# Kernel optimization log

Measured on AMD Instinct MI355X. Metric: run time of the kernel, lower is better.

## Reference

```python
import jax, jax.numpy as jnp
import numpy as np
from jax import lax

H = 32  # input_size == hidden_size
NUM_CLASSES = 10


def setup_inputs() -> dict:
    key = jax.random.key(0)
    ks = jax.random.split(key, 12)
    s = 1.0 / np.sqrt(H)  # torch default uniform(-1/sqrt(H), 1/sqrt(H))
    u = lambda k, shape: jax.random.uniform(k, shape, jnp.float32, -s, s)
    return {
        "x": jax.random.normal(ks[0], (512, 2048, H), jnp.float32),
        "W_ih0": u(ks[1], (H, H)),
        "W_hh0": u(ks[2], (H, H)),
        "b_ih0": u(ks[3], (H,)),
        "b_hh0": u(ks[4], (H,)),
        "W_ih1": u(ks[5], (H, H)),
        "W_hh1": u(ks[6], (H, H)),
        "b_ih1": u(ks[7], (H,)),
        "b_hh1": u(ks[8], (H,)),
        "fc_w": u(ks[9], (NUM_CLASSES, H)),
        "fc_b": u(ks[10], (NUM_CLASSES,)),
    }


def reference(x, W_ih0, W_hh0, b_ih0, b_hh0, W_ih1, W_hh1, b_ih1, b_hh1, fc_w, fc_b):
    # x: [B, T, H]; 2-layer tanh RNN, return logits from final hidden of layer 2.
    B = x.shape[0]
    h0 = jnp.zeros((B, H), x.dtype)

    def step(carry, x_t):
        h1, h2 = carry
        h1 = jnp.tanh(x_t @ W_ih0.T + b_ih0 + h1 @ W_hh0.T + b_hh0)
        h2 = jnp.tanh(h1 @ W_ih1.T + b_ih1 + h2 @ W_hh1.T + b_hh1)
        return (h1, h2), None

    xT = jnp.swapaxes(x, 0, 1)  # [T, B, H] for scan over time
    (_, h2_final), _ = lax.scan(step, (h0, h0), xT)
    return h2_final @ fc_w.T + fc_b  # [B, NUM_CLASSES]
```

## Files before the change

kernel.cpp:

```cpp
#include <hip/hip_runtime.h>

#define RH 32
#define RT 2048
#define RB 512
#define RC 10

#define XRING 0
#define H1OFF 512
#define H2OFF 544
#define TRASH 576
#define LDSF  608

__device__ __forceinline__ float fast_tanh(float x) {
    float e = __builtin_amdgcn_exp2f(x * 2.88539008177792681472f);
    return fmaf(-2.0f, __builtin_amdgcn_rcpf(e + 1.0f), 1.0f);
}

__global__ __launch_bounds__(64) void rnn2_kernel(
    const float* __restrict__ x,
    const float* __restrict__ W_ih0, const float* __restrict__ W_hh0,
    const float* __restrict__ b_ih0, const float* __restrict__ b_hh0,
    const float* __restrict__ W_ih1, const float* __restrict__ W_hh1,
    const float* __restrict__ b_ih1, const float* __restrict__ b_hh1,
    const float* __restrict__ fc_w, const float* __restrict__ fc_b,
    float* __restrict__ out)
{
    __shared__ float lds[LDSF];
    const int b    = blockIdx.x;
    const int lane = threadIdx.x;
    const int j    = lane & 31;
    const int half = lane >> 5;

    const float* WA = half ? W_hh1 : W_hh0;
    const float* WB = half ? W_ih1 : W_ih0;
    float wa[RH], wb[RH];
#pragma unroll
    for (int q = 0; q < 8; ++q) {
        float4 va = *(const float4*)&WA[j * RH + q * 4];
        float4 vb = *(const float4*)&WB[j * RH + q * 4];
        wa[q*4+0]=va.x; wa[q*4+1]=va.y; wa[q*4+2]=va.z; wa[q*4+3]=va.w;
        wb[q*4+0]=vb.x; wb[q*4+1]=vb.y; wb[q*4+2]=vb.z; wb[q*4+3]=vb.w;
    }
    const float bias = half ? (b_ih1[j] + b_hh1[j]) : (b_ih0[j] + b_hh0[j]);

    if (lane < RH) { lds[H1OFF + lane] = 0.0f; lds[H2OFF + lane] = 0.0f; }
    __syncthreads();

    const float* pA  = &lds[half ? H2OFF : H1OFF];
    const float* ph1 = &lds[H1OFF];
    float* wr_norm   = &lds[(half ? H2OFF : H1OFF) + j];
    float* wr_first  = half ? &lds[TRASH + j] : &lds[H1OFF + j];
    float* wr_last   = half ? &lds[H2OFF + j] : &lds[TRASH + j];

    const float* xg = x + (size_t)b * RT * RH + lane * 4;
#define STAGE(c)  __builtin_amdgcn_global_load_lds( \
        (const __attribute__((address_space(1))) void*)(xg + (c) * 256), \
        (__attribute__((address_space(3))) void*)&lds[XRING + ((c) & 1) * 256], \
        16, 0, 0)

#define STEP(XB, S, WRP) do {                                                \
        const float4* Af = (const float4*)pA;                                \
        const float4* Bf = (const float4*)(half ? ph1 : ((XB) + (S) * RH));  \
        float sA0=0.f,sA1=0.f,sA2=0.f,sA3=0.f;                               \
        float sB0=0.f,sB1=0.f,sB2=0.f,sB3=0.f;                               \
        _Pragma("unroll")                                                    \
        for (int q = 0; q < 4; ++q) {                                        \
            float4 a0 = Af[q], a1 = Af[q+4];                                 \
            float4 b0 = Bf[q], b1 = Bf[q+4];                                 \
            sA0 = fmaf(wa[q*4+0], a0.x, sA0);                                \
            sA1 = fmaf(wa[q*4+1], a0.y, sA1);                                \
            sA2 = fmaf(wa[q*4+2], a0.z, sA2);                                \
            sA3 = fmaf(wa[q*4+3], a0.w, sA3);                                \
            sA0 = fmaf(wa[16+q*4+0], a1.x, sA0);                             \
            sA1 = fmaf(wa[16+q*4+1], a1.y, sA1);                             \
            sA2 = fmaf(wa[16+q*4+2], a1.z, sA2);                             \
            sA3 = fmaf(wa[16+q*4+3], a1.w, sA3);                             \
            sB0 = fmaf(wb[q*4+0], b0.x, sB0);                                \
            sB1 = fmaf(wb[q*4+1], b0.y, sB1);                                \
            sB2 = fmaf(wb[q*4+2], b0.z, sB2);                                \
            sB3 = fmaf(wb[q*4+3], b0.w, sB3);                                \
            sB0 = fmaf(wb[16+q*4+0], b1.x, sB0);                             \
            sB1 = fmaf(wb[16+q*4+1], b1.y, sB1);                             \
            sB2 = fmaf(wb[16+q*4+2], b1.z, sB2);                             \
            sB3 = fmaf(wb[16+q*4+3], b1.w, sB3);                             \
        }                                                                    \
        float r = ((sA0+sA1)+(sA2+sA3)) + ((sB0+sB1)+(sB2+sB3));             \
        *(WRP) = fast_tanh(r + bias);                                        \
        __asm__ volatile("" ::: "memory");                                   \
    } while (0)

    STAGE(0);
    STAGE(1);

    STAGE(2);
    __asm__ volatile("s_waitcnt vmcnt(2)" ::: "memory");
    {
        const float* xb = &lds[XRING];
        STEP(xb, 0, wr_first);
        STEP(xb, 1, wr_norm); STEP(xb, 2, wr_norm); STEP(xb, 3, wr_norm);
        STEP(xb, 4, wr_norm); STEP(xb, 5, wr_norm); STEP(xb, 6, wr_norm);
        STEP(xb, 7, wr_norm);
    }
    for (int c = 1; c <= 253; ++c) {
        STAGE(c + 2);
        __asm__ volatile("s_waitcnt vmcnt(2)" ::: "memory");
        const float* xb = &lds[XRING + (c & 1) * 256];
        STEP(xb, 0, wr_norm); STEP(xb, 1, wr_norm); STEP(xb, 2, wr_norm);
        STEP(xb, 3, wr_norm); STEP(xb, 4, wr_norm); STEP(xb, 5, wr_norm);
        STEP(xb, 6, wr_norm); STEP(xb, 7, wr_norm);
    }
    __asm__ volatile("s_waitcnt vmcnt(1)" ::: "memory");
    {
        const float* xb = &lds[XRING];
        STEP(xb, 0, wr_norm); STEP(xb, 1, wr_norm); STEP(xb, 2, wr_norm);
        STEP(xb, 3, wr_norm); STEP(xb, 4, wr_norm); STEP(xb, 5, wr_norm);
        STEP(xb, 6, wr_norm); STEP(xb, 7, wr_norm);
    }
    __asm__ volatile("s_waitcnt vmcnt(0)" ::: "memory");
    {
        const float* xb = &lds[XRING + 256];
        STEP(xb, 0, wr_norm); STEP(xb, 1, wr_norm); STEP(xb, 2, wr_norm);
        STEP(xb, 3, wr_norm); STEP(xb, 4, wr_norm); STEP(xb, 5, wr_norm);
        STEP(xb, 6, wr_norm); STEP(xb, 7, wr_norm);
    }
    {
        const float* xb = &lds[XRING];
        STEP(xb, 0, wr_last);
    }
#undef STEP
#undef STAGE

    if (lane < RC) {
        float s = fc_b[lane];
#pragma unroll
        for (int k = 0; k < RH; ++k)
            s = fmaf(fc_w[lane * RH + k], lds[H2OFF + k], s);
        out[b * RC + lane] = s;
    }
}

extern "C" void kernel_launch(void* const* d_in, const int* in_sizes, int n_in,
                              void* d_out, int out_size, void* d_ws, size_t ws_size,
                              hipStream_t stream) {
    const float* x     = (const float*)d_in[0];
    const float* W_ih0 = (const float*)d_in[1];
    const float* W_hh0 = (const float*)d_in[2];
    const float* b_ih0 = (const float*)d_in[3];
    const float* b_hh0 = (const float*)d_in[4];
    const float* W_ih1 = (const float*)d_in[5];
    const float* W_hh1 = (const float*)d_in[6];
    const float* b_ih1 = (const float*)d_in[7];
    const float* b_hh1 = (const float*)d_in[8];
    const float* fc_w  = (const float*)d_in[9];
    const float* fc_b  = (const float*)d_in[10];
    float* out = (float*)d_out;

    rnn2_kernel<<<RB, 64, 0, stream>>>(x, W_ih0, W_hh0, b_ih0, b_hh0,
                                       W_ih1, W_hh1, b_ih1, b_hh1,
                                       fc_w, fc_b, out);
}
```

Before: 484.8 us.

## Rewrite RNN recurrence with bf16 split-precision MFMA over 16-sequence batches

The per-sequence scalar FMA kernel is replaced by one that packs 16 batch rows per block and computes each step's matvecs with 16x16x32 bf16 MFMA instructions. Weights and hidden states are split into hi/lo bf16 pairs to keep near-fp32 accuracy, though x is rounded to a single bf16. Layer 1 and layer 2 run on separate wavefronts in a software pipeline, exchanging h1 through LDS with a block barrier every step. The grid drops from 512 blocks to 32, so most CUs sit idle, and the serial chain now pays MFMA latency plus a barrier per timestep.

```diff
diff --git a/kernel.cpp b/kernel.cpp
--- a/kernel.cpp
+++ b/kernel.cpp
@@ -2,21 +2,39 @@
 
 #define RH 32
 #define RT 2048
-#define RB 512
 #define RC 10
 
-#define XRING 0
-#define H1OFF 512
-#define H2OFF 544
-#define TRASH 576
-#define LDSF  608
-
+typedef __attribute__((ext_vector_type(8))) short bf16x8;
+typedef __attribute__((ext_vector_type(4))) float f32x4;
+
+#define MFMA(a,b,c) __builtin_amdgcn_mfma_f32_16x16x32_bf16((a),(b),(c),0,0,0)
+
+__device__ __forceinline__ unsigned short f2bf(float f) {
+    unsigned u = __float_as_uint(f);
+    u += 0x7fffu + ((u >> 16) & 1u);
+    return (unsigned short)(u >> 16);
+}
+__device__ __forceinline__ float bf2f(unsigned short h) {
+    return __uint_as_float(((unsigned)h) << 16);
+}
 __device__ __forceinline__ float fast_tanh(float x) {
     float e = __builtin_amdgcn_exp2f(x * 2.88539008177792681472f);
     return fmaf(-2.0f, __builtin_amdgcn_rcpf(e + 1.0f), 1.0f);
 }
 
-__global__ __launch_bounds__(64) void rnn2_kernel(
+__device__ __forceinline__ void load_wfrag(const float* __restrict__ W, int base,
+                                           int n, int g, bf16x8& hi, bf16x8& lo) {
+#pragma unroll
+    for (int e = 0; e < 8; ++e) {
+        int k = 4*g + (e & 3) + 16*(e >> 2);
+        float w = W[(base + n)*RH + k];
+        unsigned short hb = f2bf(w);
+        hi[e] = (short)hb;
+        lo[e] = (short)f2bf(w - bf2f(hb));
+    }
+}
+
+__global__ __launch_bounds__(128) void rnn2_mfma_kernel(
     const float* __restrict__ x,
     const float* __restrict__ W_ih0, const float* __restrict__ W_hh0,
     const float* __restrict__ b_ih0, const float* __restrict__ b_hh0,
@@ -25,118 +43,152 @@
     const float* __restrict__ fc_w, const float* __restrict__ fc_b,
     float* __restrict__ out)
 {
-    __shared__ float lds[LDSF];
-    const int b    = blockIdx.x;
-    const int lane = threadIdx.x;
-    const int j    = lane & 31;
-    const int half = lane >> 5;
-
-    const float* WA = half ? W_hh1 : W_hh0;
-    const float* WB = half ? W_ih1 : W_ih0;
-    float wa[RH], wb[RH];
-#pragma unroll
-    for (int q = 0; q < 8; ++q) {
-        float4 va = *(const float4*)&WA[j * RH + q * 4];
-        float4 vb = *(const float4*)&WB[j * RH + q * 4];
-        wa[q*4+0]=va.x; wa[q*4+1]=va.y; wa[q*4+2]=va.z; wa[q*4+3]=va.w;
-        wb[q*4+0]=vb.x; wb[q*4+1]=vb.y; wb[q*4+2]=vb.z; wb[q*4+3]=vb.w;
-    }
-    const float bias = half ? (b_ih1[j] + b_hh1[j]) : (b_ih0[j] + b_hh0[j]);
-
-    if (lane < RH) { lds[H1OFF + lane] = 0.0f; lds[H2OFF + lane] = 0.0f; }
-    __syncthreads();
-
-    const float* pA  = &lds[half ? H2OFF : H1OFF];
-    const float* ph1 = &lds[H1OFF];
-    float* wr_norm   = &lds[(half ? H2OFF : H1OFF) + j];
-    float* wr_first  = half ? &lds[TRASH + j] : &lds[H1OFF + j];
-    float* wr_last   = half ? &lds[H2OFF + j] : &lds[TRASH + j];
-
-    const float* xg = x + (size_t)b * RT * RH + lane * 4;
-#define STAGE(c)  __builtin_amdgcn_global_load_lds( \
-        (const __attribute__((address_space(1))) void*)(xg + (c) * 256), \
-        (__attribute__((address_space(3))) void*)&lds[XRING + ((c) & 1) * 256], \
-        16, 0, 0)
-
-#define STEP(XB, S, WRP) do {                                                \
-        const float4* Af = (const float4*)pA;                                \
-        const float4* Bf = (const float4*)(half ? ph1 : ((XB) + (S) * RH));  \
-        float sA0=0.f,sA1=0.f,sA2=0.f,sA3=0.f;                               \
-        float sB0=0.f,sB1=0.f,sB2=0.f,sB3=0.f;                               \
-        _Pragma("unroll")                                                    \
-        for (int q = 0; q < 4; ++q) {                                        \
-            float4 a0 = Af[q], a1 = Af[q+4];                                 \
-            float4 b0 = Bf[q], b1 = Bf[q+4];                                 \
-            sA0 = fmaf(wa[q*4+0], a0.x, sA0);                                \
-            sA1 = fmaf(wa[q*4+1], a0.y, sA1);                                \
-            sA2 = fmaf(wa[q*4+2], a0.z, sA2);                                \
-            sA3 = fmaf(wa[q*4+3], a0.w, sA3);                                \
-            sA0 = fmaf(wa[16+q*4+0], a1.x, sA0);                             \
-            sA1 = fmaf(wa[16+q*4+1], a1.y, sA1);                             \
-            sA2 = fmaf(wa[16+q*4+2], a1.z, sA2);                             \
-            sA3 = fmaf(wa[16+q*4+3], a1.w, sA3);                             \
-            sB0 = fmaf(wb[q*4+0], b0.x, sB0);                                \
-            sB1 = fmaf(wb[q*4+1], b0.y, sB1);                                \
-            sB2 = fmaf(wb[q*4+2], b0.z, sB2);                                \
-            sB3 = fmaf(wb[q*4+3], b0.w, sB3);                                \
-            sB0 = fmaf(wb[16+q*4+0], b1.x, sB0);                             \
-            sB1 = fmaf(wb[16+q*4+1], b1.y, sB1);                             \
-            sB2 = fmaf(wb[16+q*4+2], b1.z, sB2);                             \
-            sB3 = fmaf(wb[16+q*4+3], b1.w, sB3);                             \
-        }                                                                    \
-        float r = ((sA0+sA1)+(sA2+sA3)) + ((sB0+sB1)+(sB2+sB3));             \
-        *(WRP) = fast_tanh(r + bias);                                        \
-        __asm__ volatile("" ::: "memory");                                   \
-    } while (0)
-
-    STAGE(0);
-    STAGE(1);
-
-    STAGE(2);
-    __asm__ volatile("s_waitcnt vmcnt(2)" ::: "memory");
-    {
-        const float* xb = &lds[XRING];
-        STEP(xb, 0, wr_first);
-        STEP(xb, 1, wr_norm); STEP(xb, 2, wr_norm); STEP(xb, 3, wr_norm);
-        STEP(xb, 4, wr_norm); STEP(xb, 5, wr_norm); STEP(xb, 6, wr_norm);
-        STEP(xb, 7, wr_norm);
-    }
-    for (int c = 1; c <= 253; ++c) {
-        STAGE(c + 2);
-        __asm__ volatile("s_waitcnt vmcnt(2)" ::: "memory");
-        const float* xb = &lds[XRING + (c & 1) * 256];
-        STEP(xb, 0, wr_norm); STEP(xb, 1, wr_norm); STEP(xb, 2, wr_norm);
-        STEP(xb, 3, wr_norm); STEP(xb, 4, wr_norm); STEP(xb, 5, wr_norm);
-        STEP(xb, 6, wr_norm); STEP(xb, 7, wr_norm);
-    }
-    __asm__ volatile("s_waitcnt vmcnt(1)" ::: "memory");
-    {
-        const float* xb = &lds[XRING];
-        STEP(xb, 0, wr_norm); STEP(xb, 1, wr_norm); STEP(xb, 2, wr_norm);
-        STEP(xb, 3, wr_norm); STEP(xb, 4, wr_norm); STEP(xb, 5, wr_norm);
-        STEP(xb, 6, wr_norm); STEP(xb, 7, wr_norm);
-    }
-    __asm__ volatile("s_waitcnt vmcnt(0)" ::: "memory");
-    {
-        const float* xb = &lds[XRING + 256];
-        STEP(xb, 0, wr_norm); STEP(xb, 1, wr_norm); STEP(xb, 2, wr_norm);
-        STEP(xb, 3, wr_norm); STEP(xb, 4, wr_norm); STEP(xb, 5, wr_norm);
-        STEP(xb, 6, wr_norm); STEP(xb, 7, wr_norm);
-    }
-    {
-        const float* xb = &lds[XRING];
-        STEP(xb, 0, wr_last);
-    }
-#undef STEP
-#undef STAGE
-
-    if (lane < RC) {
-        float s = fc_b[lane];
-#pragma unroll
-        for (int k = 0; k < RH; ++k)
-            s = fmaf(fc_w[lane * RH + k], lds[H2OFF + k], s);
-        out[b * RC + lane] = s;
-    }
+    __shared__ __align__(16) short hslab[2][2][64][8];
+    __shared__ __align__(16) float h2fin[16][RH];
+
+    const int tid = threadIdx.x;
+    const int wv  = tid >> 6;
+    const int ln  = tid & 63;
+    const int n   = ln & 15;
+    const int g   = ln >> 4;
+
+    bf16x8 WIhi0, WIlo0, WIhi1, WIlo1;
+    bf16x8 WHhi0, WHlo0, WHhi1, WHlo1;
+    bf16x8 hsh = {0,0,0,0,0,0,0,0};
+    bf16x8 hsl = {0,0,0,0,0,0,0,0};
+    f32x4 cba, cbb;
+
+    if (wv == 0) {
+        load_wfrag(W_ih0,  0, n, g, WIhi0, WIlo0);
+        load_wfrag(W_ih0, 16, n, g, WIhi1, WIlo1);
+        load_wfrag(W_hh0,  0, n, g, WHhi0, WHlo0);
+        load_wfrag(W_hh0, 16, n, g, WHhi1, WHlo1);
+#pragma unroll
+        for (int i = 0; i < 4; ++i) {
+            cba[i] = b_ih0[4*g + i]      + b_hh0[4*g + i];
+            cbb[i] = b_ih0[16 + 4*g + i] + b_hh0[16 + 4*g + i];
+        }
+    } else {
+        load_wfrag(W_ih1,  0, n, g, WIhi0, WIlo0);
+        load_wfrag(W_ih1, 16, n, g, WIhi1, WIlo1);
+        load_wfrag(W_hh1,  0, n, g, WHhi0, WHlo0);
+        load_wfrag(W_hh1, 16, n, g, WHhi1, WHlo1);
+#pragma unroll
+        for (int i = 0; i < 4; ++i) {
+            cba[i] = b_ih1[4*g + i]      + b_hh1[4*g + i];
+            cbb[i] = b_ih1[16 + 4*g + i] + b_hh1[16 + 4*g + i];
+        }
+    }
+
+    const float* xbase = x + (size_t)(blockIdx.x*16 + n) * (RT*RH) + 4*g;
+    float4 xa0, xb0, xa1, xb1, xa2, xb2, xa3, xb3;
+
+#define PREF(XA, XB, TP) do { \
+    int tp_ = (TP); if (tp_ > RT-1) tp_ = RT-1; \
+    const float* p_ = xbase + tp_*RH; \
+    XA = *(const float4*)(p_); \
+    XB = *(const float4*)(p_ + 16); \
+} while (0)
+
+#define TANH4(dst, dv) do { dst[0]=fast_tanh(dv[0]); dst[1]=fast_tanh(dv[1]); \
+                            dst[2]=fast_tanh(dv[2]); dst[3]=fast_tanh(dv[3]); } while(0)
+
+#define PACKH(t0_, t1_) do { \
+    _Pragma("unroll") \
+    for (int e_ = 0; e_ < 8; ++e_) { \
+        float v_ = (e_ < 4) ? t0_[e_ & 3] : t1_[e_ & 3]; \
+        unsigned short hb_ = f2bf(v_); \
+        hsh[e_] = (short)hb_; \
+        hsl[e_] = (short)f2bf(v_ - bf2f(hb_)); \
+    } \
+} while (0)
+
+#define ASTEP(T_, XA, XB, WSL, DOPREF) do { \
+    bf16x8 xf_; \
+    xf_[0]=(short)f2bf(XA.x); xf_[1]=(short)f2bf(XA.y); \
+    xf_[2]=(short)f2bf(XA.z); xf_[3]=(short)f2bf(XA.w); \
+    xf_[4]=(short)f2bf(XB.x); xf_[5]=(short)f2bf(XB.y); \
+    xf_[6]=(short)f2bf(XB.z); xf_[7]=(short)f2bf(XB.w); \
+    if (DOPREF) { PREF(XA, XB, (T_) + 4); } \
+    f32x4 d0_, d1_; \
+    d0_ = MFMA(WIhi0, xf_, cba);  d1_ = MFMA(WIhi1, xf_, cbb); \
+    d0_ = MFMA(WIlo0, xf_, d0_);  d1_ = MFMA(WIlo1, xf_, d1_); \
+    d0_ = MFMA(WHhi0, hsh, d0_);  d1_ = MFMA(WHhi1, hsh, d1_); \
+    d0_ = MFMA(WHhi0, hsl, d0_);  d1_ = MFMA(WHhi1, hsl, d1_); \
+    d0_ = MFMA(WHlo0, hsh, d0_);  d1_ = MFMA(WHlo1, hsh, d1_); \
+    float t0_[4], t1_[4]; TANH4(t0_, d0_); TANH4(t1_, d1_); \
+    PACKH(t0_, t1_); \
+    *(bf16x8*)&hslab[WSL][0][ln][0] = hsh; \
+    *(bf16x8*)&hslab[WSL][1][ln][0] = hsl; \
+} while (0)
+
+#define BSTEP(RSL, FIN) do { \
+    bf16x8 rhi_ = *(const bf16x8*)&hslab[RSL][0][ln][0]; \
+    bf16x8 rlo_ = *(const bf16x8*)&hslab[RSL][1][ln][0]; \
+    f32x4 d0_, d1_; \
+    d0_ = MFMA(WIhi0, rhi_, cba);  d1_ = MFMA(WIhi1, rhi_, cbb); \
+    d0_ = MFMA(WIhi0, rlo_, d0_);  d1_ = MFMA(WIhi1, rlo_, d1_); \
+    d0_ = MFMA(WIlo0, rhi_, d0_);  d1_ = MFMA(WIlo1, rhi_, d1_); \
+    d0_ = MFMA(WHhi0, hsh, d0_);   d1_ = MFMA(WHhi1, hsh, d1_); \
+    d0_ = MFMA(WHhi0, hsl, d0_);   d1_ = MFMA(WHhi1, hsl, d1_); \
+    d0_ = MFMA(WHlo0, hsh, d0_);   d1_ = MFMA(WHlo1, hsh, d1_); \
+    float t0_[4], t1_[4]; TANH4(t0_, d0_); TANH4(t1_, d1_); \
+    if (FIN) { \
+        f32x4 o0_, o1_; \
+        o0_[0]=t0_[0]; o0_[1]=t0_[1]; o0_[2]=t0_[2]; o0_[3]=t0_[3]; \
+        o1_[0]=t1_[0]; o1_[1]=t1_[1]; o1_[2]=t1_[2]; o1_[3]=t1_[3]; \
+        *(f32x4*)&h2fin[n][4*g]      = o0_; \
+        *(f32x4*)&h2fin[n][16 + 4*g] = o1_; \
+    } else { \
+        PACKH(t0_, t1_); \
+    } \
+} while (0)
+
+    if (wv == 0) {
+        PREF(xa0, xb0, 0); PREF(xa1, xb1, 1);
+        PREF(xa2, xb2, 2); PREF(xa3, xb3, 3);
+        ASTEP(0, xa0, xb0, 0, 1);
+    }
+    __syncthreads();
+
+    for (int k = 0; k < 511; ++k) {
+        const int tb = 4*k;
+        if (wv == 0) ASTEP(tb+1, xa1, xb1, 1, 1); else BSTEP(0, 0);
+        __syncthreads();
+        if (wv == 0) ASTEP(tb+2, xa2, xb2, 0, 1); else BSTEP(1, 0);
+        __syncthreads();
+        if (wv == 0) ASTEP(tb+3, xa3, xb3, 1, 1); else BSTEP(0, 0);
+        __syncthreads();
+        if (wv == 0) ASTEP(tb+4, xa0, xb0, 0, 1); else BSTEP(1, 0);
+        __syncthreads();
+    }
+    if (wv == 0) ASTEP(2045, xa1, xb1, 1, 0); else BSTEP(0, 0);
+    __syncthreads();
+    if (wv == 0) ASTEP(2046, xa2, xb2, 0, 0); else BSTEP(1, 0);
+    __syncthreads();
+    if (wv == 0) ASTEP(2047, xa3, xb3, 1, 0); else BSTEP(0, 0);
+    __syncthreads();
+
+    if (wv == 1) {
+        BSTEP(1, 1);
+        const int batch = blockIdx.x * 16 + n;
+#pragma unroll
+        for (int ci = 0; ci < 3; ++ci) {
+            int cc = g + 4*ci;
+            if (cc < RC) {
+                float s = fc_b[cc];
+#pragma unroll
+                for (int kk = 0; kk < RH; ++kk)
+                    s = fmaf(fc_w[cc*RH + kk], h2fin[n][kk], s);
+                out[batch*RC + cc] = s;
+            }
+        }
+    }
+#undef PREF
+#undef TANH4
+#undef PACKH
+#undef ASTEP
+#undef BSTEP
 }
 
 extern "C" void kernel_launch(void* const* d_in, const int* in_sizes, int n_in,
@@ -155,7 +207,7 @@
     const float* fc_b  = (const float*)d_in[10];
     float* out = (float*)d_out;
 
-    rnn2_kernel<<<RB, 64, 0, stream>>>(x, W_ih0, W_hh0, b_ih0, b_hh0,
-                                       W_ih1, W_hh1, b_ih1, b_hh1,
-                                       fc_w, fc_b, out);
-}
+    rnn2_mfma_kernel<<<32, 128, 0, stream>>>(x, W_ih0, W_hh0, b_ih0, b_hh0,
+                                             W_ih1, W_hh1, b_ih1, b_hh1,
+                                             fc_w, fc_b, out);
+}
```

Result: slower. 863.7 us (+78.2%).
